# Performance work log

Measured on AMD Instinct MI355X. Metric: run time of the kernel, lower is better.

The kernel has to match this reference:

```python
import jax, jax.numpy as jnp
import numpy as np

B, S, E, H, N = 16384, 256, 128, 128, 34  # batch, state_dim, reduced_lang_dim, mlp hidden, N_task
TEMP = 0.1
EPS = 1e-8  # torch cosine_similarity eps


def setup_inputs() -> dict:
    key = jax.random.key(0)
    ks = jax.random.split(key, 12)
    sc = 0.05
    return {
        "state": jax.random.normal(ks[0], (B, S), dtype=jnp.float32),
        "task_id": jax.random.randint(ks[1], (B,), 0, N),
        "prior": jax.random.normal(ks[2], (B, N), dtype=jnp.float32),
        # stacked weights of the 34 per-task MLPs (Linear(S,H) -> ReLU -> Linear(H,H) -> ReLU -> Linear(H,E))
        "W1": jax.random.normal(ks[3], (N, S, H), dtype=jnp.float32) * sc,
        "b1": jax.random.normal(ks[4], (N, H), dtype=jnp.float32) * sc,
        "W2": jax.random.normal(ks[5], (N, H, H), dtype=jnp.float32) * sc,
        "b2": jax.random.normal(ks[6], (N, H), dtype=jnp.float32) * sc,
        "W3": jax.random.normal(ks[7], (N, H, E), dtype=jnp.float32) * sc,
        "b3": jax.random.normal(ks[8], (N, E), dtype=jnp.float32) * sc,
        "lang_emb": jax.random.normal(ks[9], (N, E), dtype=jnp.float32),
    }


def reference(state, task_id, prior, W1, b1, W2, b2, W3, b3, lang_emb):
    # 34 parallel MLPs as a single batched GEMM stack: [B,S] x [N,S,H] -> [B,N,H]
    h = jax.nn.relu(jnp.einsum('bs,nsh->bnh', state, W1) + b1)
    h = jax.nn.relu(jnp.einsum('bnh,nhk->bnk', h, W2) + b2)
    q = jnp.einsum('bnk,nke->bne', h, W3) + b3            # [B,N,E]
    # normalize (torch.norm division, no eps, then cosine_similarity renormalizes -> unit)
    q = q / jnp.linalg.norm(q, axis=-1, keepdims=True)
    lang = lang_emb[task_id]                              # [B,E]
    lang_n = lang / jnp.maximum(jnp.linalg.norm(lang, axis=-1, keepdims=True), EPS)
    cos_sim = jnp.einsum('bne,be->bn', q, lang_n)         # [B,N]
    log_task_prob = jax.nn.log_softmax(cos_sim / TEMP, axis=-1)
    task_prob_prior = jax.nn.softmax(prior, axis=-1)      # exp(log_softmax(prior))
    latent_vec = jnp.einsum('bne,bn->be', q, task_prob_prior)
    latent_target = jax.lax.stop_gradient(q[jnp.arange(B), task_id])  # detach
    rep_vec = jnp.concatenate([state, latent_vec], axis=-1)           # [B, S+E]
    return rep_vec, log_task_prob, latent_target, latent_vec
```

## Files before the change

kernel.cpp:

```cpp
#include <hip/hip_runtime.h>
#include <hip/hip_bf16.h>
#include <hip/hip_fp16.h>
#include <cstdint>
#include <cstddef>

typedef __bf16 bf16;
typedef __attribute__((ext_vector_type(8))) __bf16 bf16x8;
typedef __attribute__((ext_vector_type(16))) float f32x16;

static_assert(sizeof(bf16x8) == 16, "bf16x8 must be 16B");

#define NTASK 34
#define BTOT 16384
#define WSTRIDE 73728

__device__ __forceinline__ f32x16 mfma32(bf16x8 a, bf16x8 b, f32x16 c) {
  return __builtin_amdgcn_mfma_f32_32x32x16_bf16(a, b, c, 0, 0, 0);
}

__device__ __forceinline__ void gload_lds16(const void* g, void* l) {
  __builtin_amdgcn_global_load_lds((__attribute__((address_space(1))) void*)g,
                                   (__attribute__((address_space(3))) void*)l,
                                   16, 0, 0);
}

__device__ __forceinline__ unsigned pack2(float lo, float hi) {
  union { __bf16 h[2]; unsigned u; } v;
  v.h[0] = (__bf16)lo; v.h[1] = (__bf16)hi;
  return v.u;
}

__device__ __forceinline__ void pl32swap(unsigned &a, unsigned &b) {
  asm volatile("v_permlane32_swap_b32 %0, %1" : "+v"(a), "+v"(b));
}

__global__ void prep_all(const float* __restrict__ W1, const float* __restrict__ W2,
                         const float* __restrict__ W3, const float* __restrict__ b1,
                         const float* __restrict__ b2, const float* __restrict__ b3,
                         const float* __restrict__ state, const float* __restrict__ prior,
                         bf16* __restrict__ wdst, bf16* __restrict__ sdst,
                         float* __restrict__ ppt) {
  int bid = blockIdx.x;
  if (bid < 1224) {
    int idx = bid * 256 + threadIdx.x;
    int n = idx / 9216;
    int r = idx - n * 9216;
    int g = r >> 8;
    int m = (r >> 6) & 3;
    int l = r & 63;
    int col = m * 32 + (l & 31);
    int kj = (l >> 5) << 3;
    bf16x8 v;
#pragma unroll
    for (int j = 0; j < 8; ++j) v[j] = (bf16)0.f;
    if (g < 16) {
      const float* s = W1 + ((size_t)n * 256 + g * 16 + kj) * 128 + col;
#pragma unroll
      for (int j = 0; j < 8; ++j) v[j] = (bf16)s[(size_t)j * 128];
    } else if (g == 16) {
      if (l < 32) v[0] = (bf16)b1[n * 128 + col];
    } else if (g == 17) {
    } else if (g < 26) {
      const float* s = W2 + ((size_t)n * 128 + (g - 18) * 16 + kj) * 128 + col;
#pragma unroll
      for (int j = 0; j < 8; ++j) v[j] = (bf16)s[(size_t)j * 128];
    } else if (g == 26) {
      if (l < 32) v[0] = (bf16)b2[n * 128 + col];
    } else if (g < 35) {
      const float* s = W3 + ((size_t)n * 128 + (g - 27) * 16 + kj) * 128 + col;
#pragma unroll
      for (int j = 0; j < 8; ++j) v[j] = (bf16)s[(size_t)j * 128];
    } else {
      if (l < 32) v[0] = (bf16)b3[n * 128 + col];
    }
    *(bf16x8*)(wdst + (size_t)n * WSTRIDE + (size_t)(g * 4 + m) * 512 + l * 8) = v;
  } else if (bid < 3272) {
    int idx = (bid - 1224) * 256 + threadIdx.x;
    int rb = idx >> 10;
    int r = idx & 1023;
    int ks = r >> 6;
    int l = r & 63;
    int b = rb * 32 + (l & 31);
    int k0 = ks * 16 + ((l >> 5) << 3);
    const float* s = state + (size_t)b * 256 + k0;
    bf16x8 v;
#pragma unroll
    for (int j = 0; j < 8; ++j) v[j] = (bf16)s[j];
    *(bf16x8*)(sdst + (size_t)(rb * 16 + ks) * 512 + l * 8) = v;
  } else {
    int row = (bid - 3272) * 4 + (threadIdx.x >> 6);
    int lane = threadIdx.x & 63;
    float v = (lane < NTASK) ? prior[(size_t)row * NTASK + lane] : -INFINITY;
    float m = v;
#pragma unroll
    for (int mm = 1; mm < 64; mm <<= 1) m = fmaxf(m, __shfl_xor(m, mm));
    float e = (lane < NTASK) ? expf(v - m) : 0.0f;
    float s = e;
#pragma unroll
    for (int mm = 1; mm < 64; mm <<= 1) s += __shfl_xor(s, mm);
    if (lane < NTASK) ppt[(size_t)lane * BTOT + row] = e / s;
  }
}

__global__ void prep_langn(const float* __restrict__ lang, float* __restrict__ out) {
  __shared__ float red[2];
  int n = blockIdx.x;
  int t = threadIdx.x;
  float v = lang[(size_t)n * 128 + t];
  float ss = v * v;
#pragma unroll
  for (int m = 1; m < 64; m <<= 1) ss += __shfl_xor(ss, m);
  if ((t & 63) == 0) red[t >> 6] = ss;
  __syncthreads();
  float s = red[0] + red[1];
  float sc = 1.0f / fmaxf(sqrtf(s), 1e-8f);
  out[(size_t)n * 128 + t] = v * sc;
}


__global__ void __launch_bounds__(256, 3)
pass1_kernel(const int* __restrict__ task_id, const bf16* __restrict__ wstream,
             const bf16* __restrict__ sf, const float* __restrict__ langn,
             const float* __restrict__ pp_t,
             float* __restrict__ cs_t, __half* __restrict__ lat_part,
             float* __restrict__ out_tgt) {
  __shared__ __align__(16) bf16 shW[24576];

  const int tid = threadIdx.x;
  const int l = tid & 63;
  const int wid = tid >> 6;
  const int hi = l >> 5;
  const int b = l & 31;
  const int tg = blockIdx.x >> 7;
  const int rg = blockIdx.x & 127;
  const int start = (tg < 4) ? tg * 6 : (24 + (tg - 4) * 5);
  const int cnt = (tg < 4) ? 6 : 5;
  const int row0 = rg * 128 + wid * 32 + b;
  const int rb0 = rg * 4 + wid;

  const int tidn = task_id[row0];
  const bf16* sb = sf + (size_t)rb0 * 8192 + l * 8;

#define STAGE_WIN(slot, srcoff) \
  { _Pragma("unroll") \
    for (int c = 0; c < 6; ++c) \
      gload_lds16(wstream + (srcoff) + c * 2048 + tid * 8, \
                  shW + (slot) * 12288 + c * 2048 + tid * 8); }

#define WIN_TOP() \
  { asm volatile("s_waitcnt vmcnt(0)" ::: "memory"); \
    __builtin_amdgcn_s_barrier(); }

#define KMFMA(slot, gl, bop) \
  { _Pragma("unroll") \
    for (int mt = 0; mt < 4; ++mt) { \
      bf16x8 wf = *(const bf16x8*)(shW + (slot) * 12288 + ((gl) * 4 + mt) * 512 + l * 8); \
      acc[mt] = mfma32(wf, (bop), acc[mt]); } }

  STAGE_WIN(0, (size_t)start * WSTRIDE);
  bf16x8 sring[4];
#pragma unroll
  for (int i = 0; i < 4; ++i) sring[i] = *(const bf16x8*)(sb + i * 512);

  union { unsigned u[4]; bf16x8 v; } cf;
  cf.u[0] = (l < 32) ? 0x3f80u : 0u;
  cf.u[1] = 0u; cf.u[2] = 0u; cf.u[3] = 0u;

  f32x16 z;
#pragma unroll
  for (int i = 0; i < 16; ++i) z[i] = 0.f;

  const __half2 hz = __float2half2_rn(0.0f);
  __half2 lat[4][4][2];
#pragma unroll
  for (int mt = 0; mt < 4; ++mt)
#pragma unroll
    for (int q = 0; q < 4; ++q) { lat[mt][q][0] = hz; lat[mt][q][1] = hz; }

  auto transition = [&](f32x16* acc, bf16x8* f) {
#pragma unroll
    for (int mt = 0; mt < 4; ++mt) {
      unsigned p[8];
#pragma unroll
      for (int q = 0; q < 4; ++q) {
        p[2 * q]     = pack2(fmaxf(acc[mt][4 * q + 0], 0.f), fmaxf(acc[mt][4 * q + 1], 0.f));
        p[2 * q + 1] = pack2(fmaxf(acc[mt][4 * q + 2], 0.f), fmaxf(acc[mt][4 * q + 3], 0.f));
      }
      pl32swap(p[0], p[2]); pl32swap(p[1], p[3]);
      pl32swap(p[4], p[6]); pl32swap(p[5], p[7]);
      union { unsigned u[4]; bf16x8 v; } e, o;
      e.u[0] = p[0]; e.u[1] = p[1]; e.u[2] = p[2]; e.u[3] = p[3];
      o.u[0] = p[4]; o.u[1] = p[5]; o.u[2] = p[6]; o.u[3] = p[7];
      f[2 * mt] = e.v; f[2 * mt + 1] = o.v;
    }
  };

  for (int t = 0; t < cnt; ++t) {
    const int n = start + t;
    const size_t wb = (size_t)n * WSTRIDE;
    f32x16 acc[4];
    bf16x8 f2[8], f3[8];

    WIN_TOP();
    STAGE_WIN(1, wb + 12288);
#pragma unroll
    for (int mt = 0; mt < 4; ++mt) acc[mt] = z;
    __builtin_amdgcn_s_setprio(1);
#pragma unroll
    for (int gl = 0; gl < 6; ++gl) {
      bf16x8 sv = sring[gl & 3];
      sring[gl & 3] = *(const bf16x8*)(sb + (gl + 4) * 512);
      KMFMA(0, gl, sv);
    }
    __builtin_amdgcn_s_setprio(0);

    WIN_TOP();
    STAGE_WIN(0, wb + 24576);
    __builtin_amdgcn_s_setprio(1);
#pragma unroll
    for (int gl = 0; gl < 6; ++gl) {
      int ks = 6 + gl;
      bf16x8 sv = sring[ks & 3];
      sring[ks & 3] = *(const bf16x8*)(sb + (ks + 4) * 512);
      KMFMA(1, gl, sv);
    }
    __builtin_amdgcn_s_setprio(0);

    WIN_TOP();
    STAGE_WIN(1, wb + 36864);
    __builtin_amdgcn_s_setprio(1);
#pragma unroll
    for (int gl = 0; gl < 4; ++gl) {
      int ks = 12 + gl;
      KMFMA(0, gl, sring[ks & 3]);
    }
    KMFMA(0, 4, cf.v);
    __builtin_amdgcn_s_setprio(0);
    transition(acc, f2);

    WIN_TOP();
    STAGE_WIN(0, wb + 49152);
#pragma unroll
    for (int mt = 0; mt < 4; ++mt) acc[mt] = z;
    __builtin_amdgcn_s_setprio(1);
#pragma unroll
    for (int gl = 0; gl < 6; ++gl) KMFMA(1, gl, f2[gl]);
    __builtin_amdgcn_s_setprio(0);

    WIN_TOP();
    STAGE_WIN(1, wb + 61440);
    __builtin_amdgcn_s_setprio(1);
    KMFMA(0, 0, f2[6]);
    KMFMA(0, 1, f2[7]);
    KMFMA(0, 2, cf.v);
    __builtin_amdgcn_s_setprio(0);
    transition(acc, f3);
#pragma unroll
    for (int mt = 0; mt < 4; ++mt) acc[mt] = z;
    __builtin_amdgcn_s_setprio(1);
    KMFMA(0, 3, f3[0]);
    KMFMA(0, 4, f3[1]);
    KMFMA(0, 5, f3[2]);
    __builtin_amdgcn_s_setprio(0);

    WIN_TOP();
    if (t + 1 < cnt) {
      STAGE_WIN(0, wb + WSTRIDE);
#pragma unroll
      for (int i = 0; i < 4; ++i) sring[i] = *(const bf16x8*)(sb + i * 512);
    }
    __builtin_amdgcn_s_setprio(1);
#pragma unroll
    for (int gl = 0; gl < 5; ++gl) KMFMA(1, gl, f3[3 + gl]);
    KMFMA(1, 5, cf.v);
    __builtin_amdgcn_s_setprio(0);

    float ssq = 0.f, dot = 0.f;
    const float* lgb = langn + (size_t)tidn * 128;
#pragma unroll
    for (int mt = 0; mt < 4; ++mt)
#pragma unroll
      for (int q = 0; q < 4; ++q) {
        int c0 = mt * 32 + q * 8 + 4 * hi;
        float4 lg = *(const float4*)(lgb + c0);
        float a0 = acc[mt][4 * q + 0], a1 = acc[mt][4 * q + 1];
        float a2 = acc[mt][4 * q + 2], a3 = acc[mt][4 * q + 3];
        ssq += a0 * a0 + a1 * a1 + a2 * a2 + a3 * a3;
        dot += a0 * lg.x + a1 * lg.y + a2 * lg.z + a3 * lg.w;
      }
    ssq += __shfl_xor(ssq, 32);
    dot += __shfl_xor(dot, 32);
    float inv = rsqrtf(ssq);
    if (l < 32) cs_t[(size_t)row0 * NTASK + n] = dot * inv;
    float pwi = pp_t[(size_t)n * BTOT + row0] * inv;
    __half2 pw2 = __float2half2_rn(pwi);
#pragma unroll
    for (int mt = 0; mt < 4; ++mt)
#pragma unroll
      for (int q = 0; q < 4; ++q) {
        lat[mt][q][0] = __hfma2(__floats2half2_rn(acc[mt][4 * q + 0], acc[mt][4 * q + 1]),
                                pw2, lat[mt][q][0]);
        lat[mt][q][1] = __hfma2(__floats2half2_rn(acc[mt][4 * q + 2], acc[mt][4 * q + 3]),
                                pw2, lat[mt][q][1]);
      }
    if (tidn == n) {
#pragma unroll
      for (int mt = 0; mt < 4; ++mt)
#pragma unroll
        for (int q = 0; q < 4; ++q) {
          float4 qv = {acc[mt][4 * q + 0] * inv, acc[mt][4 * q + 1] * inv,
                       acc[mt][4 * q + 2] * inv, acc[mt][4 * q + 3] * inv};
          *(float4*)(out_tgt + (size_t)row0 * 128 + mt * 32 + q * 8 + 4 * hi) = qv;
        }
    }
  }

  __half* lp = lat_part + ((size_t)tg * BTOT + row0) * 128;
#pragma unroll
  for (int mt = 0; mt < 4; ++mt)
#pragma unroll
    for (int q = 0; q < 4; ++q) {
      int c0 = mt * 32 + q * 8 + 4 * hi;
      union { __half2 h[2]; uint2 u; } v;
      v.h[0] = lat[mt][q][0];
      v.h[1] = lat[mt][q][1];
      *(uint2*)(lp + c0) = v.u;
    }
#undef STAGE_WIN
#undef WIN_TOP
#undef KMFMA
}


__global__ void __launch_bounds__(256)
pass3_kernel(const float* __restrict__ state, const float* __restrict__ cs_t,
             const __half* __restrict__ lat_part,
             float* __restrict__ out_rep, float* __restrict__ out_ltp,
             float* __restrict__ out_lat) {
  int w = threadIdx.x >> 6, l = threadIdx.x & 63;
  size_t row = (size_t)blockIdx.x * 4 + w;

  float c = (l < NTASK) ? cs_t[row * NTASK + l] * 10.0f : -1e30f;
  float cm = c;
#pragma unroll
  for (int mm = 1; mm < 64; mm <<= 1) cm = fmaxf(cm, __shfl_xor(cm, mm));
  float ce = (l < NTASK) ? expf(c - cm) : 0.0f;
  float cs = ce;
#pragma unroll
  for (int mm = 1; mm < 64; mm <<= 1) cs += __shfl_xor(cs, mm);
  if (l < NTASK) out_ltp[row * NTASK + l] = c - cm - logf(cs);

  float2 lv = {0.f, 0.f};
#pragma unroll
  for (int g = 0; g < 6; ++g) {
    __half2 p = *(const __half2*)(lat_part + ((size_t)g * BTOT + row) * 128 + 2 * l);
    lv.x += __low2float(p);
    lv.y += __high2float(p);
  }
  *(float2*)(out_lat + row * 128 + 2 * l) = lv;
  *(float2*)(out_rep + row * 384 + 256 + 2 * l) = lv;

  float4 sv = *(const float4*)(state + row * 256 + l * 4);
  *(float4*)(out_rep + row * 384 + l * 4) = sv;
}


extern "C" void kernel_launch(void* const* d_in, const int* in_sizes, int n_in,
                              void* d_out, int out_size, void* d_ws, size_t ws_size,
                              hipStream_t stream) {
  (void)in_sizes; (void)n_in; (void)out_size; (void)ws_size;
  const float* state = (const float*)d_in[0];
  const int* task_id = (const int*)d_in[1];
  const float* prior = (const float*)d_in[2];
  const float* W1 = (const float*)d_in[3];
  const float* b1 = (const float*)d_in[4];
  const float* W2 = (const float*)d_in[5];
  const float* b2 = (const float*)d_in[6];
  const float* W3 = (const float*)d_in[7];
  const float* b3 = (const float*)d_in[8];
  const float* lang = (const float*)d_in[9];

  char* ws = (char*)d_ws;
  bf16* wstream  = (bf16*)(ws + 0);
  bf16* sf       = (bf16*)(ws + 5013504);
  float* langn   = (float*)(ws + 13402112);
  float* pp_t    = (float*)(ws + 13419520);
  float* cs_t    = (float*)(ws + 15647744);
  __half* lat_part = (__half*)(ws + 17875968);

  float* out = (float*)d_out;
  float* out_rep = out;
  float* out_ltp = out + 6291456;
  float* out_tgt = out + 6848512;
  float* out_lat = out + 8945664;

  prep_all<<<7368, 256, 0, stream>>>(W1, W2, W3, b1, b2, b3, state, prior,
                                     wstream, sf, pp_t);
  prep_langn<<<NTASK, 128, 0, stream>>>(lang, langn);
  pass1_kernel<<<768, 256, 0, stream>>>(task_id, wstream, sf, langn, pp_t,
                                        cs_t, lat_part, out_tgt);
  pass3_kernel<<<4096, 256, 0, stream>>>(state, cs_t, lat_part,
                                         out_rep, out_ltp, out_lat);
}
```

Baseline: 166.1 us.

## Triple-buffer weight windows and split tasks across eight groups

Restructures pass1's weight streaming from two 12K-element windows into three 8K-element LDS slots, with partial vmcnt waits so two windows stay in flight. Tasks are split into 8 groups of 4-5 instead of 6 groups of 5-6, raising the grid from 768 to 1024 blocks. pass3 now reduces 8 partials. The latent accumulator moves from packed half to fp32 registers, and launch bounds drop to 2 blocks per SM to leave room for those registers. The cost is higher register pressure, lower occupancy, and more partial-sum traffic in exchange for deeper prefetch and better precision.

Result: faster. 145.1 us (-12.7%).

```diff
diff --git a/kernel.cpp b/kernel.cpp
--- a/kernel.cpp
+++ b/kernel.cpp
@@ -118,13 +118,13 @@
 }
 
 
-__global__ void __launch_bounds__(256, 3)
+__global__ void __launch_bounds__(256, 2)
 pass1_kernel(const int* __restrict__ task_id, const bf16* __restrict__ wstream,
              const bf16* __restrict__ sf, const float* __restrict__ langn,
              const float* __restrict__ pp_t,
              float* __restrict__ cs_t, __half* __restrict__ lat_part,
              float* __restrict__ out_tgt) {
-  __shared__ __align__(16) bf16 shW[24576];
+  __shared__ __align__(16) bf16 shW[3 * 8192];
 
   const int tid = threadIdx.x;
   const int l = tid & 63;
@@ -133,34 +133,37 @@
   const int b = l & 31;
   const int tg = blockIdx.x >> 7;
   const int rg = blockIdx.x & 127;
-  const int start = (tg < 4) ? tg * 6 : (24 + (tg - 4) * 5);
-  const int cnt = (tg < 4) ? 6 : 5;
+  const int start = tg * 4 + (tg < 2 ? tg : 2);
+  const int cnt = 4 + (tg < 2 ? 1 : 0);
+  const int nwin = cnt * 9;
   const int row0 = rg * 128 + wid * 32 + b;
   const int rb0 = rg * 4 + wid;
 
   const int tidn = task_id[row0];
   const bf16* sb = sf + (size_t)rb0 * 8192 + l * 8;
-
-#define STAGE_WIN(slot, srcoff) \
+  const bf16* wsrc = wstream + (size_t)start * WSTRIDE;
+
+#define STAGE_WIN(slot, w) \
   { _Pragma("unroll") \
-    for (int c = 0; c < 6; ++c) \
-      gload_lds16(wstream + (srcoff) + c * 2048 + tid * 8, \
-                  shW + (slot) * 12288 + c * 2048 + tid * 8); }
-
-#define WIN_TOP() \
-  { asm volatile("s_waitcnt vmcnt(0)" ::: "memory"); \
+    for (int c = 0; c < 4; ++c) \
+      gload_lds16(wsrc + (size_t)(w) * 8192 + c * 2048 + tid * 8, \
+                  shW + (slot) * 8192 + c * 2048 + tid * 8); }
+
+#define WIN_TOP(N) \
+  { asm volatile("s_waitcnt vmcnt(" #N ")" ::: "memory"); \
     __builtin_amdgcn_s_barrier(); }
 
-#define KMFMA(slot, gl, bop) \
+#define KMFMA(slot, gi, bop) \
   { _Pragma("unroll") \
     for (int mt = 0; mt < 4; ++mt) { \
-      bf16x8 wf = *(const bf16x8*)(shW + (slot) * 12288 + ((gl) * 4 + mt) * 512 + l * 8); \
+      bf16x8 wf = *(const bf16x8*)(shW + (slot) * 8192 + ((gi) * 4 + mt) * 512 + l * 8); \
       acc[mt] = mfma32(wf, (bop), acc[mt]); } }
 
-  STAGE_WIN(0, (size_t)start * WSTRIDE);
-  bf16x8 sring[4];
-#pragma unroll
-  for (int i = 0; i < 4; ++i) sring[i] = *(const bf16x8*)(sb + i * 512);
+  STAGE_WIN(0, 0);
+  STAGE_WIN(1, 1);
+  bf16x8 sring[8];
+#pragma unroll
+  for (int i = 0; i < 8; ++i) sring[i] = *(const bf16x8*)(sb + i * 512);
 
   union { unsigned u[4]; bf16x8 v; } cf;
   cf.u[0] = (l < 32) ? 0x3f80u : 0u;
@@ -169,13 +172,7 @@
   f32x16 z;
 #pragma unroll
   for (int i = 0; i < 16; ++i) z[i] = 0.f;
-
-  const __half2 hz = __float2half2_rn(0.0f);
-  __half2 lat[4][4][2];
-#pragma unroll
-  for (int mt = 0; mt < 4; ++mt)
-#pragma unroll
-    for (int q = 0; q < 4; ++q) { lat[mt][q][0] = hz; lat[mt][q][1] = hz; }
+  f32x16 lat[4] = {z, z, z, z};
 
   auto transition = [&](f32x16* acc, bf16x8* f) {
 #pragma unroll
@@ -197,58 +194,66 @@
 
   for (int t = 0; t < cnt; ++t) {
     const int n = start + t;
-    const size_t wb = (size_t)n * WSTRIDE;
+    const int w0g = t * 9;
     f32x16 acc[4];
     bf16x8 f2[8], f3[8];
 
-    WIN_TOP();
-    STAGE_WIN(1, wb + 12288);
+    WIN_TOP(12);
+    if (w0g + 2 < nwin) STAGE_WIN(2, w0g + 2);
 #pragma unroll
     for (int mt = 0; mt < 4; ++mt) acc[mt] = z;
     __builtin_amdgcn_s_setprio(1);
 #pragma unroll
-    for (int gl = 0; gl < 6; ++gl) {
-      bf16x8 sv = sring[gl & 3];
-      sring[gl & 3] = *(const bf16x8*)(sb + (gl + 4) * 512);
-      KMFMA(0, gl, sv);
-    }
-    __builtin_amdgcn_s_setprio(0);
-
-    WIN_TOP();
-    STAGE_WIN(0, wb + 24576);
-    __builtin_amdgcn_s_setprio(1);
-#pragma unroll
-    for (int gl = 0; gl < 6; ++gl) {
-      int ks = 6 + gl;
-      bf16x8 sv = sring[ks & 3];
-      sring[ks & 3] = *(const bf16x8*)(sb + (ks + 4) * 512);
-      KMFMA(1, gl, sv);
-    }
-    __builtin_amdgcn_s_setprio(0);
-
-    WIN_TOP();
-    STAGE_WIN(1, wb + 36864);
-    __builtin_amdgcn_s_setprio(1);
-#pragma unroll
-    for (int gl = 0; gl < 4; ++gl) {
-      int ks = 12 + gl;
-      KMFMA(0, gl, sring[ks & 3]);
-    }
-    KMFMA(0, 4, cf.v);
+    for (int gi = 0; gi < 4; ++gi) KMFMA(0, gi, sring[gi]);
+    __builtin_amdgcn_s_setprio(0);
+
+    WIN_TOP(12);
+    if (w0g + 3 < nwin) STAGE_WIN(0, w0g + 3);
+#pragma unroll
+    for (int i = 0; i < 4; ++i) sring[i] = *(const bf16x8*)(sb + (8 + i) * 512);
+    __builtin_amdgcn_s_setprio(1);
+#pragma unroll
+    for (int gi = 0; gi < 4; ++gi) KMFMA(1, gi, sring[4 + gi]);
+    __builtin_amdgcn_s_setprio(0);
+
+    WIN_TOP(8);
+    if (w0g + 4 < nwin) STAGE_WIN(1, w0g + 4);
+#pragma unroll
+    for (int i = 0; i < 4; ++i) sring[4 + i] = *(const bf16x8*)(sb + (12 + i) * 512);
+    __builtin_amdgcn_s_setprio(1);
+#pragma unroll
+    for (int gi = 0; gi < 4; ++gi) KMFMA(2, gi, sring[gi]);
+    __builtin_amdgcn_s_setprio(0);
+
+    WIN_TOP(12);
+    if (w0g + 5 < nwin) STAGE_WIN(2, w0g + 5);
+    __builtin_amdgcn_s_setprio(1);
+#pragma unroll
+    for (int gi = 0; gi < 4; ++gi) KMFMA(0, gi, sring[4 + gi]);
+    __builtin_amdgcn_s_setprio(0);
+
+    WIN_TOP(8);
+    if (w0g + 6 < nwin) STAGE_WIN(0, w0g + 6);
+    __builtin_amdgcn_s_setprio(1);
+    KMFMA(1, 0, cf.v);
     __builtin_amdgcn_s_setprio(0);
     transition(acc, f2);
-
-    WIN_TOP();
-    STAGE_WIN(0, wb + 49152);
 #pragma unroll
     for (int mt = 0; mt < 4; ++mt) acc[mt] = z;
     __builtin_amdgcn_s_setprio(1);
-#pragma unroll
-    for (int gl = 0; gl < 6; ++gl) KMFMA(1, gl, f2[gl]);
-    __builtin_amdgcn_s_setprio(0);
-
-    WIN_TOP();
-    STAGE_WIN(1, wb + 61440);
+    KMFMA(1, 2, f2[0]);
+    KMFMA(1, 3, f2[1]);
+    __builtin_amdgcn_s_setprio(0);
+
+    WIN_TOP(4);
+    if (w0g + 7 < nwin) STAGE_WIN(1, w0g + 7);
+    __builtin_amdgcn_s_setprio(1);
+#pragma unroll
+    for (int gi = 0; gi < 4; ++gi) KMFMA(2, gi, f2[2 + gi]);
+    __builtin_amdgcn_s_setprio(0);
+
+    WIN_TOP(4);
+    if (w0g + 8 < nwin) STAGE_WIN(2, w0g + 8);
     __builtin_amdgcn_s_setprio(1);
     KMFMA(0, 0, f2[6]);
     KMFMA(0, 1, f2[7]);
@@ -259,21 +264,28 @@
     for (int mt = 0; mt < 4; ++mt) acc[mt] = z;
     __builtin_amdgcn_s_setprio(1);
     KMFMA(0, 3, f3[0]);
-    KMFMA(0, 4, f3[1]);
-    KMFMA(0, 5, f3[2]);
-    __builtin_amdgcn_s_setprio(0);
-
-    WIN_TOP();
+    __builtin_amdgcn_s_setprio(0);
+
+    WIN_TOP(4);
+    if (w0g + 9 < nwin) STAGE_WIN(0, w0g + 9);
+    __builtin_amdgcn_s_setprio(1);
+#pragma unroll
+    for (int gi = 0; gi < 4; ++gi) KMFMA(1, gi, f3[1 + gi]);
+    __builtin_amdgcn_s_setprio(0);
+
+    WIN_TOP(4);
+    if (w0g + 10 < nwin) STAGE_WIN(1, w0g + 10);
+    __builtin_amdgcn_s_setprio(1);
+    KMFMA(2, 0, f3[5]);
+    KMFMA(2, 1, f3[6]);
+    KMFMA(2, 2, f3[7]);
+    KMFMA(2, 3, cf.v);
+    __builtin_amdgcn_s_setprio(0);
+
     if (t + 1 < cnt) {
-      STAGE_WIN(0, wb + WSTRIDE);
-#pragma unroll
-      for (int i = 0; i < 4; ++i) sring[i] = *(const bf16x8*)(sb + i * 512);
+#pragma unroll
+      for (int i = 0; i < 8; ++i) sring[i] = *(const bf16x8*)(sb + i * 512);
     }
-    __builtin_amdgcn_s_setprio(1);
-#pragma unroll
-    for (int gl = 0; gl < 5; ++gl) KMFMA(1, gl, f3[3 + gl]);
-    KMFMA(1, 5, cf.v);
-    __builtin_amdgcn_s_setprio(0);
 
     float ssq = 0.f, dot = 0.f;
     const float* lgb = langn + (size_t)tidn * 128;
@@ -293,16 +305,8 @@
     float inv = rsqrtf(ssq);
     if (l < 32) cs_t[(size_t)row0 * NTASK + n] = dot * inv;
     float pwi = pp_t[(size_t)n * BTOT + row0] * inv;
-    __half2 pw2 = __float2half2_rn(pwi);
-#pragma unroll
-    for (int mt = 0; mt < 4; ++mt)
-#pragma unroll
-      for (int q = 0; q < 4; ++q) {
-        lat[mt][q][0] = __hfma2(__floats2half2_rn(acc[mt][4 * q + 0], acc[mt][4 * q + 1]),
-                                pw2, lat[mt][q][0]);
-        lat[mt][q][1] = __hfma2(__floats2half2_rn(acc[mt][4 * q + 2], acc[mt][4 * q + 3]),
-                                pw2, lat[mt][q][1]);
-      }
+#pragma unroll
+    for (int mt = 0; mt < 4; ++mt) lat[mt] += acc[mt] * pwi;
     if (tidn == n) {
 #pragma unroll
       for (int mt = 0; mt < 4; ++mt)
@@ -321,9 +325,11 @@
 #pragma unroll
     for (int q = 0; q < 4; ++q) {
       int c0 = mt * 32 + q * 8 + 4 * hi;
-      union { __half2 h[2]; uint2 u; } v;
-      v.h[0] = lat[mt][q][0];
-      v.h[1] = lat[mt][q][1];
+      union { __half h[4]; uint2 u; } v;
+      v.h[0] = __float2half(lat[mt][4 * q + 0]);
+      v.h[1] = __float2half(lat[mt][4 * q + 1]);
+      v.h[2] = __float2half(lat[mt][4 * q + 2]);
+      v.h[3] = __float2half(lat[mt][4 * q + 3]);
       *(uint2*)(lp + c0) = v.u;
     }
 #undef STAGE_WIN
@@ -352,7 +358,7 @@
 
   float2 lv = {0.f, 0.f};
 #pragma unroll
-  for (int g = 0; g < 6; ++g) {
+  for (int g = 0; g < 8; ++g) {
     __half2 p = *(const __half2*)(lat_part + ((size_t)g * BTOT + row) * 128 + 2 * l);
     lv.x += __low2float(p);
     lv.y += __high2float(p);
@@ -397,8 +403,8 @@
   prep_all<<<7368, 256, 0, stream>>>(W1, W2, W3, b1, b2, b3, state, prior,
                                      wstream, sf, pp_t);
   prep_langn<<<NTASK, 128, 0, stream>>>(lang, langn);
-  pass1_kernel<<<768, 256, 0, stream>>>(task_id, wstream, sf, langn, pp_t,
-                                        cs_t, lat_part, out_tgt);
+  pass1_kernel<<<1024, 256, 0, stream>>>(task_id, wstream, sf, langn, pp_t,
+                                         cs_t, lat_part, out_tgt);
   pass3_kernel<<<4096, 256, 0, stream>>>(state, cs_t, lat_part,
                                          out_rep, out_ltp, out_lat);
 }
```
